# Optimization experiments

Measured on AMD Instinct MI355X. Metric: run time of the kernel, lower is better.

## Reference

```python
import jax, jax.numpy as jnp
import numpy as np

N_NODES = 100000
K_HOPS = 2


def _gcn_norm(edge_index, edge_weight, num_nodes, fill_value=1.0):
    # renorm trick: add self-loops with weight fill_value, then D^-1/2 A D^-1/2
    row, col = edge_index[0], edge_index[1]
    sl = jnp.arange(num_nodes, dtype=edge_index.dtype)
    row = jnp.concatenate([row, sl])
    col = jnp.concatenate([col, sl])
    w = jnp.concatenate([edge_weight, jnp.full((num_nodes,), fill_value, edge_weight.dtype)])
    deg = jax.ops.segment_sum(w, row, num_segments=num_nodes)
    dinv = jnp.where(deg > 0, jax.lax.rsqrt(deg), 0.0)
    normed_w = dinv[row] * w * dinv[col]
    return row, col, normed_w


def setup_inputs() -> dict:
    key = jax.random.key(0)
    k1, k2, k3 = jax.random.split(key, 3)
    n_edges, d, units = 1000000, 64, 64
    x = jax.random.normal(k1, (N_NODES, d), dtype=jnp.float32)
    edge_index = jax.random.randint(k2, (2, n_edges), 0, N_NODES, dtype=jnp.int32)
    edge_weight = jnp.ones((n_edges,), dtype=jnp.float32)
    kernel = jax.random.normal(k3, (d, units), dtype=jnp.float32) * (1.0 / np.sqrt(d))
    bias = jnp.zeros((units,), dtype=jnp.float32)
    return {"x": x, "edge_index": edge_index, "edge_weight": edge_weight,
            "kernel": kernel, "bias": bias}


def reference(x, edge_index, edge_weight, kernel, bias):
    # SGC: K-hop normalized sparse propagation, then single dense linear
    row, col, w = _gcn_norm(edge_index, edge_weight, N_NODES, fill_value=1.0)
    h = x
    for _ in range(K_HOPS):
        h = jax.ops.segment_sum(w[:, None] * h[col], row, num_segments=N_NODES)
    out = h @ kernel + bias  # activation=None
    return out
```

## Files before the change

### kernel.cpp

```cpp
#include <hip/hip_runtime.h>


constexpr int kN = 100000;
constexpr int kD = 64;
constexpr int BSHIFT = 9;
constexpr int NBUCK = (kN + 511) >> BSHIFT;
constexpr int CHUNK = 4096;
constexpr int XW_ROWS = 128;

__device__ __forceinline__ float bf2f(unsigned short u) {
    return __uint_as_float(((unsigned)u) << 16);
}
__device__ __forceinline__ unsigned short f2bf(float f) {
    unsigned b = __float_as_uint(f);
    b += 0x7FFF + ((b >> 16) & 1);
    return (unsigned short)(b >> 16);
}

__global__ __launch_bounds__(256) void kA_count(const int* __restrict__ row,
                                                int* __restrict__ bc, int nblk, int E) {
    __shared__ int hist[256];
    int t = threadIdx.x;
    hist[t] = 0;
    __syncthreads();
    int g0 = blockIdx.x * CHUNK;
    int n = min(CHUNK, E - g0);
    for (int i = t; i < n; i += 256) {
        atomicAdd(&hist[row[g0 + i] >> BSHIFT], 1);
    }
    __syncthreads();
    if (t < NBUCK) bc[t * nblk + blockIdx.x] = hist[t];
}

__global__ __launch_bounds__(256) void kA_scanB(int* __restrict__ bc,
                                                int* __restrict__ tot, int nblk) {
    __shared__ int sh[256];
    int b = blockIdx.x;
    int t = threadIdx.x;
    int* p = bc + (size_t)b * nblk;
    int ipt = (nblk + 255) >> 8;
    int s0 = t * ipt;
    int s1 = min(s0 + ipt, nblk);
    int lsum = 0;
    for (int k = s0; k < s1; ++k) lsum += p[k];
    sh[t] = lsum;
    __syncthreads();
    for (int off = 1; off < 256; off <<= 1) {
        int add = (t >= off) ? sh[t - off] : 0;
        __syncthreads();
        sh[t] += add;
        __syncthreads();
    }
    int run = sh[t] - lsum;
    for (int k = s0; k < s1; ++k) {
        int v = p[k];
        p[k] = run;
        run += v;
    }
    if (t == 255) tot[b] = sh[255];
}

__global__ __launch_bounds__(256) void kA_scanT(const int* __restrict__ tot,
                                                int* __restrict__ base) {
    __shared__ int sh[256];
    int t = threadIdx.x;
    int v = (t < NBUCK) ? tot[t] : 0;
    sh[t] = v;
    __syncthreads();
    for (int off = 1; off < 256; off <<= 1) {
        int add = (t >= off) ? sh[t - off] : 0;
        __syncthreads();
        sh[t] += add;
        __syncthreads();
    }
    if (t < NBUCK) base[t] = sh[t] - v;
}

__global__ __launch_bounds__(256) void kA_place(const int* __restrict__ row,
                                                const int* __restrict__ col,
                                                const float* __restrict__ w,
                                                const int* __restrict__ bc,
                                                const int* __restrict__ base, int nblk,
                                                int2* __restrict__ tmp, int E) {
    __shared__ int hist[256];
    __shared__ int lbase[256];
    __shared__ int gb[256];
    __shared__ int cur[256];
    __shared__ int2 stage[CHUNK];
    __shared__ unsigned char bkt[CHUNK];
    int t = threadIdx.x;
    hist[t] = 0;
    __syncthreads();
    int g0 = blockIdx.x * CHUNK;
    int n = min(CHUNK, E - g0);
    for (int i = t; i < n; i += 256) {
        atomicAdd(&hist[row[g0 + i] >> BSHIFT], 1);
    }
    __syncthreads();
    int v = hist[t];
    lbase[t] = v;
    __syncthreads();
    for (int off = 1; off < 256; off <<= 1) {
        int add = (t >= off) ? lbase[t - off] : 0;
        __syncthreads();
        lbase[t] += add;
        __syncthreads();
    }
    int excl = lbase[t] - v;
    __syncthreads();
    lbase[t] = excl;
    cur[t] = excl;
    if (t < NBUCK) gb[t] = base[t] + bc[t * nblk + blockIdx.x];
    __syncthreads();
    for (int i = t; i < n; i += 256) {
        int r = row[g0 + i];
        int c = col[g0 + i];
        float wv = w[g0 + i];
        int b = r >> BSHIFT;
        int lp = atomicAdd(&cur[b], 1);
        stage[lp] = make_int2(c | ((r & 511) << 17), __float_as_int(wv));
        bkt[lp] = (unsigned char)b;
    }
    __syncthreads();
    for (int i = t; i < n; i += 256) {
        int b = bkt[i];
        tmp[gb[b] + (i - lbase[b])] = stage[i];
    }
}

__global__ __launch_bounds__(512) void kB_sort(const int2* __restrict__ tmp,
                                               const int* __restrict__ base,
                                               int2* __restrict__ ecw,
                                               int* __restrict__ start,
                                               float* __restrict__ dinv, int E) {
    __shared__ int hist[512];
    __shared__ int lstart[512];
    __shared__ int cur[512];
    int b = blockIdx.x;
    int t = threadIdx.x;
    int gbase = base[b];
    int gend = (b == NBUCK - 1) ? E : base[b + 1];
    int size = gend - gbase;
    int node0 = b << BSHIFT;
    int nloc = min(512, kN - node0);
    hist[t] = 0;
    __syncthreads();
    for (int i = t; i < size; i += 512) {
        atomicAdd(&hist[(tmp[gbase + i].x >> 17) & 511], 1);
    }
    __syncthreads();
    int v = hist[t];
    lstart[t] = v;
    __syncthreads();
    for (int off = 1; off < 512; off <<= 1) {
        int add = (t >= off) ? lstart[t - off] : 0;
        __syncthreads();
        lstart[t] += add;
        __syncthreads();
    }
    int excl = lstart[t] - v;
    __syncthreads();
    lstart[t] = excl;
    cur[t] = excl;
    __syncthreads();
    if (t < nloc) start[node0 + t] = gbase + excl;
    if (b == 0 && t == 0) start[kN] = E;
    for (int i = t; i < size; i += 512) {
        int2 e = tmp[gbase + i];
        int rl = (e.x >> 17) & 511;
        int lp = atomicAdd(&cur[rl], 1);
        ecw[gbase + lp] = e;
    }
    __syncthreads();
    if (t < nloc) {
        int s = gbase + lstart[t];
        int eend = s + hist[t];
        float d = 1.0f;
        for (int j = s; j < eend; ++j) d += __int_as_float(ecw[j].y);
        dinv[node0 + t] = (d > 0.0f) ? rsqrtf(d) : 0.0f;
    }
}

__global__ __launch_bounds__(256) void k_norm(const int* __restrict__ base,
                                              const float* __restrict__ dinv,
                                              int2* __restrict__ ecw, int E) {
    int b = blockIdx.x;
    int gbase = base[b];
    int gend = (b == NBUCK - 1) ? E : base[b + 1];
    int node0 = b << BSHIFT;
    for (int i = gbase + threadIdx.x; i < gend; i += 256) {
        int2 v = ecw[i];
        int c = v.x & 0x1FFFF;
        int rl = (v.x >> 17) & 511;
        float wn = dinv[node0 + rl] * __int_as_float(v.y) * dinv[c];
        ecw[i] = make_int2(c << 7, __float_as_int(wn));
    }
}

__global__ __launch_bounds__(256) void k_xw(const float* __restrict__ x,
                                            const float* __restrict__ W,
                                            unsigned short* __restrict__ y, int n) {
    __shared__ float Xs[XW_ROWS][kD];
    int t = threadIdx.x;
    int lane = t & 63;
    int wv = t >> 6;
    int row0 = blockIdx.x * XW_ROWS;
    float Wc[kD];
#pragma unroll
    for (int k = 0; k < kD; ++k) Wc[k] = W[k * kD + lane];
    for (int i = t; i < XW_ROWS * (kD / 4); i += 256) {
        int r = i >> 4;
        int q = i & 15;
        float4 v = make_float4(0.0f, 0.0f, 0.0f, 0.0f);
        if (row0 + r < n)
            v = *reinterpret_cast<const float4*>(x + (size_t)(row0 + r) * kD + q * 4);
        *reinterpret_cast<float4*>(&Xs[r][q * 4]) = v;
    }
    __syncthreads();
    int rbase = wv * 32;
#pragma unroll
    for (int rr = 0; rr < 32; rr += 2) {
        int r0 = rbase + rr;
        float acc0 = 0.0f, acc1 = 0.0f;
#pragma unroll
        for (int q = 0; q < 16; ++q) {
            float4 a = *reinterpret_cast<const float4*>(&Xs[r0][q * 4]);
            float4 b = *reinterpret_cast<const float4*>(&Xs[r0 + 1][q * 4]);
            acc0 = fmaf(a.x, Wc[q * 4 + 0], acc0);
            acc1 = fmaf(b.x, Wc[q * 4 + 0], acc1);
            acc0 = fmaf(a.y, Wc[q * 4 + 1], acc0);
            acc1 = fmaf(b.y, Wc[q * 4 + 1], acc1);
            acc0 = fmaf(a.z, Wc[q * 4 + 2], acc0);
            acc1 = fmaf(b.z, Wc[q * 4 + 2], acc1);
            acc0 = fmaf(a.w, Wc[q * 4 + 3], acc0);
            acc1 = fmaf(b.w, Wc[q * 4 + 3], acc1);
        }
        int gr = row0 + r0;
        if (gr < n) y[(size_t)gr * kD + lane] = f2bf(acc0);
        if (gr + 1 < n) y[(size_t)(gr + 1) * kD + lane] = f2bf(acc1);
    }
}

template <typename OutWriter>
__device__ __forceinline__ void hop_body(const int* __restrict__ start,
                                         const int2* __restrict__ ecw,
                                         const float* __restrict__ dinv,
                                         const unsigned short* __restrict__ h_in,
                                         int n, OutWriter writeout) {
    int node = blockIdx.x * 4 + __builtin_amdgcn_readfirstlane(threadIdx.x >> 6);
    int lane = threadIdx.x & 63;
    if (node >= n) return;
    const char* hb = (const char*)h_in;
    int lo = lane << 1;
    float di = dinv[node];
    float self = bf2f(h_in[(size_t)node * kD + lane]);
    float acc = di * di * self;
    int s = start[node], e = start[node + 1];
    int j = s;
    for (; j + 7 < e; j += 8) {
        int2 v0 = ecw[j + 0], v1 = ecw[j + 1], v2 = ecw[j + 2], v3 = ecw[j + 3];
        int2 v4 = ecw[j + 4], v5 = ecw[j + 5], v6 = ecw[j + 6], v7 = ecw[j + 7];
        float g0 = bf2f(*(const unsigned short*)(hb + (unsigned)(v0.x + lo)));
        float g1 = bf2f(*(const unsigned short*)(hb + (unsigned)(v1.x + lo)));
        float g2 = bf2f(*(const unsigned short*)(hb + (unsigned)(v2.x + lo)));
        float g3 = bf2f(*(const unsigned short*)(hb + (unsigned)(v3.x + lo)));
        float g4 = bf2f(*(const unsigned short*)(hb + (unsigned)(v4.x + lo)));
        float g5 = bf2f(*(const unsigned short*)(hb + (unsigned)(v5.x + lo)));
        float g6 = bf2f(*(const unsigned short*)(hb + (unsigned)(v6.x + lo)));
        float g7 = bf2f(*(const unsigned short*)(hb + (unsigned)(v7.x + lo)));
        acc = fmaf(__int_as_float(v0.y), g0, acc);
        acc = fmaf(__int_as_float(v1.y), g1, acc);
        acc = fmaf(__int_as_float(v2.y), g2, acc);
        acc = fmaf(__int_as_float(v3.y), g3, acc);
        acc = fmaf(__int_as_float(v4.y), g4, acc);
        acc = fmaf(__int_as_float(v5.y), g5, acc);
        acc = fmaf(__int_as_float(v6.y), g6, acc);
        acc = fmaf(__int_as_float(v7.y), g7, acc);
    }
    for (; j + 3 < e; j += 4) {
        int2 v0 = ecw[j + 0], v1 = ecw[j + 1], v2 = ecw[j + 2], v3 = ecw[j + 3];
        float g0 = bf2f(*(const unsigned short*)(hb + (unsigned)(v0.x + lo)));
        float g1 = bf2f(*(const unsigned short*)(hb + (unsigned)(v1.x + lo)));
        float g2 = bf2f(*(const unsigned short*)(hb + (unsigned)(v2.x + lo)));
        float g3 = bf2f(*(const unsigned short*)(hb + (unsigned)(v3.x + lo)));
        acc = fmaf(__int_as_float(v0.y), g0, acc);
        acc = fmaf(__int_as_float(v1.y), g1, acc);
        acc = fmaf(__int_as_float(v2.y), g2, acc);
        acc = fmaf(__int_as_float(v3.y), g3, acc);
    }
    for (; j < e; ++j) {
        int2 v = ecw[j];
        acc = fmaf(__int_as_float(v.y),
                   bf2f(*(const unsigned short*)(hb + (unsigned)(v.x + lo))), acc);
    }
    writeout(node, lane, di, acc);
}

__global__ __launch_bounds__(256) void k_hop1(const int* __restrict__ start,
                                              const int2* __restrict__ ecw,
                                              const float* __restrict__ dinv,
                                              const unsigned short* __restrict__ h_in,
                                              unsigned short* __restrict__ h_out, int n) {
    hop_body(start, ecw, dinv, h_in, n,
             [=](int node, int lane, float di, float acc) {
                 h_out[(size_t)node * kD + lane] = f2bf(acc);
             });
}

__global__ __launch_bounds__(256) void k_hop2(const int* __restrict__ start,
                                              const int2* __restrict__ ecw,
                                              const float* __restrict__ dinv,
                                              const unsigned short* __restrict__ h_in,
                                              const float* __restrict__ bias,
                                              float* __restrict__ out, int n) {
    hop_body(start, ecw, dinv, h_in, n,
             [=](int node, int lane, float di, float acc) {
                 out[(size_t)node * kD + lane] = acc + bias[lane];
             });
}

extern "C" void kernel_launch(void* const* d_in, const int* in_sizes, int n_in,
                              void* d_out, int out_size, void* d_ws, size_t ws_size,
                              hipStream_t stream) {
    const float* x    = (const float*)d_in[0];
    const int*   ei   = (const int*)d_in[1];
    const float* ew   = (const float*)d_in[2];
    const float* W    = (const float*)d_in[3];
    const float* bias = (const float*)d_in[4];
    const int E = in_sizes[1] / 2;
    const int* row = ei;
    const int* col = ei + E;

    const int nblk = (E + CHUNK - 1) / CHUNK;

    char* ws = (char*)d_ws;
    auto alloc = [&](size_t bytes) {
        char* p = ws;
        ws += ((bytes + 1023) & ~(size_t)1023);
        return p;
    };
    int*            base  = (int*)alloc(sizeof(int) * 256);
    int*            tot   = (int*)alloc(sizeof(int) * 256);
    int*            bc    = (int*)alloc(sizeof(int) * (size_t)NBUCK * nblk);
    int*            start = (int*)alloc(sizeof(int) * (kN + 1));
    float*          dinv  = (float*)alloc(sizeof(float) * kN);
    int2*           ecw   = (int2*)alloc(sizeof(int2) * (size_t)E);
    unsigned short* y     = (unsigned short*)alloc(sizeof(short) * (size_t)kN * kD);
    unsigned short* h1    = (unsigned short*)alloc(sizeof(short) * (size_t)kN * kD);
    int2*           tmp   = (int2*)h1;

    k_xw<<<(kN + XW_ROWS - 1) / XW_ROWS, 256, 0, stream>>>(x, W, y, kN);

    kA_count<<<nblk, 256, 0, stream>>>(row, bc, nblk, E);
    kA_scanB<<<NBUCK, 256, 0, stream>>>(bc, tot, nblk);
    kA_scanT<<<1, 256, 0, stream>>>(tot, base);
    kA_place<<<nblk, 256, 0, stream>>>(row, col, ew, bc, base, nblk, tmp, E);
    kB_sort<<<NBUCK, 512, 0, stream>>>(tmp, base, ecw, start, dinv, E);
    k_norm<<<NBUCK, 256, 0, stream>>>(base, dinv, ecw, E);

    k_hop1<<<(kN + 3) / 4, 256, 0, stream>>>(start, ecw, dinv, y, h1, kN);
    k_hop2<<<(kN + 3) / 4, 256, 0, stream>>>(start, ecw, dinv, h1, bias,
                                             (float*)d_out, kN);
}
```

Before: 144.8 us.

## Compute degrees in a separate pass, fold edge normalization into sort, predicate hop tail

Degrees are now computed by a new per-bucket kernel that does shared-memory atomic adds over the bucketed edges. Edge normalization moves into the bucket sort's scatter, which removes the separate k_norm pass and the serial per-node degree loop that re-read ecw. The hop gather loop drops its 4-wide and scalar remainder loops in favour of a single 8-wide loop with clamped indices and zeroed weights, so short rows issue redundant but harmless loads. The final output store becomes nontemporal.

```diff
diff --git a/kernel.cpp b/kernel.cpp
--- a/kernel.cpp
+++ b/kernel.cpp
@@ -128,13 +128,35 @@
     }
 }
 
+__global__ __launch_bounds__(512) void kD_deg(const int2* __restrict__ tmp,
+                                              const int* __restrict__ base,
+                                              float* __restrict__ dinv, int E) {
+    __shared__ float degs[512];
+    int b = blockIdx.x;
+    int t = threadIdx.x;
+    degs[t] = 0.0f;
+    __syncthreads();
+    int gbase = base[b];
+    int gend = (b == NBUCK - 1) ? E : base[b + 1];
+    int node0 = b << BSHIFT;
+    int nloc = min(512, kN - node0);
+    for (int i = gbase + t; i < gend; i += 512) {
+        int2 e = tmp[i];
+        atomicAdd(&degs[(e.x >> 17) & 511], __int_as_float(e.y));
+    }
+    __syncthreads();
+    if (t < nloc) {
+        float d = 1.0f + degs[t];
+        dinv[node0 + t] = (d > 0.0f) ? rsqrtf(d) : 0.0f;
+    }
+}
+
 __global__ __launch_bounds__(512) void kB_sort(const int2* __restrict__ tmp,
                                                const int* __restrict__ base,
+                                               const float* __restrict__ dinv,
                                                int2* __restrict__ ecw,
-                                               int* __restrict__ start,
-                                               float* __restrict__ dinv, int E) {
+                                               int* __restrict__ start, int E) {
     __shared__ int hist[512];
-    __shared__ int lstart[512];
     __shared__ int cur[512];
     int b = blockIdx.x;
     int t = threadIdx.x;
@@ -150,50 +172,27 @@
     }
     __syncthreads();
     int v = hist[t];
-    lstart[t] = v;
+    hist[t] = v;
     __syncthreads();
     for (int off = 1; off < 512; off <<= 1) {
-        int add = (t >= off) ? lstart[t - off] : 0;
-        __syncthreads();
-        lstart[t] += add;
-        __syncthreads();
-    }
-    int excl = lstart[t] - v;
-    __syncthreads();
-    lstart[t] = excl;
+        int add = (t >= off) ? hist[t - off] : 0;
+        __syncthreads();
+        hist[t] += add;
+        __syncthreads();
+    }
+    int excl = hist[t] - v;
+    __syncthreads();
     cur[t] = excl;
     __syncthreads();
     if (t < nloc) start[node0 + t] = gbase + excl;
     if (b == 0 && t == 0) start[kN] = E;
     for (int i = t; i < size; i += 512) {
         int2 e = tmp[gbase + i];
+        int c = e.x & 0x1FFFF;
         int rl = (e.x >> 17) & 511;
+        float wn = dinv[node0 + rl] * __int_as_float(e.y) * dinv[c];
         int lp = atomicAdd(&cur[rl], 1);
-        ecw[gbase + lp] = e;
-    }
-    __syncthreads();
-    if (t < nloc) {
-        int s = gbase + lstart[t];
-        int eend = s + hist[t];
-        float d = 1.0f;
-        for (int j = s; j < eend; ++j) d += __int_as_float(ecw[j].y);
-        dinv[node0 + t] = (d > 0.0f) ? rsqrtf(d) : 0.0f;
-    }
-}
-
-__global__ __launch_bounds__(256) void k_norm(const int* __restrict__ base,
-                                              const float* __restrict__ dinv,
-                                              int2* __restrict__ ecw, int E) {
-    int b = blockIdx.x;
-    int gbase = base[b];
-    int gend = (b == NBUCK - 1) ? E : base[b + 1];
-    int node0 = b << BSHIFT;
-    for (int i = gbase + threadIdx.x; i < gend; i += 256) {
-        int2 v = ecw[i];
-        int c = v.x & 0x1FFFF;
-        int rl = (v.x >> 17) & 511;
-        float wn = dinv[node0 + rl] * __int_as_float(v.y) * dinv[c];
-        ecw[i] = make_int2(c << 7, __float_as_int(wn));
+        ecw[gbase + lp] = make_int2(c << 7, __float_as_int(wn));
     }
 }
 
@@ -256,10 +255,16 @@
     float self = bf2f(h_in[(size_t)node * kD + lane]);
     float acc = di * di * self;
     int s = start[node], e = start[node + 1];
-    int j = s;
-    for (; j + 7 < e; j += 8) {
-        int2 v0 = ecw[j + 0], v1 = ecw[j + 1], v2 = ecw[j + 2], v3 = ecw[j + 3];
-        int2 v4 = ecw[j + 4], v5 = ecw[j + 5], v6 = ecw[j + 6], v7 = ecw[j + 7];
+    int em1 = e - 1;
+    for (int j = s; j < e; j += 8) {
+        int2 v0 = ecw[j];
+        int2 v1 = ecw[min(j + 1, em1)];
+        int2 v2 = ecw[min(j + 2, em1)];
+        int2 v3 = ecw[min(j + 3, em1)];
+        int2 v4 = ecw[min(j + 4, em1)];
+        int2 v5 = ecw[min(j + 5, em1)];
+        int2 v6 = ecw[min(j + 6, em1)];
+        int2 v7 = ecw[min(j + 7, em1)];
         float g0 = bf2f(*(const unsigned short*)(hb + (unsigned)(v0.x + lo)));
         float g1 = bf2f(*(const unsigned short*)(hb + (unsigned)(v1.x + lo)));
         float g2 = bf2f(*(const unsigned short*)(hb + (unsigned)(v2.x + lo)));
@@ -268,30 +273,22 @@
         float g5 = bf2f(*(const unsigned short*)(hb + (unsigned)(v5.x + lo)));
         float g6 = bf2f(*(const unsigned short*)(hb + (unsigned)(v6.x + lo)));
         float g7 = bf2f(*(const unsigned short*)(hb + (unsigned)(v7.x + lo)));
-        acc = fmaf(__int_as_float(v0.y), g0, acc);
-        acc = fmaf(__int_as_float(v1.y), g1, acc);
-        acc = fmaf(__int_as_float(v2.y), g2, acc);
-        acc = fmaf(__int_as_float(v3.y), g3, acc);
-        acc = fmaf(__int_as_float(v4.y), g4, acc);
-        acc = fmaf(__int_as_float(v5.y), g5, acc);
-        acc = fmaf(__int_as_float(v6.y), g6, acc);
-        acc = fmaf(__int_as_float(v7.y), g7, acc);
-    }
-    for (; j + 3 < e; j += 4) {
-        int2 v0 = ecw[j + 0], v1 = ecw[j + 1], v2 = ecw[j + 2], v3 = ecw[j + 3];
-        float g0 = bf2f(*(const unsigned short*)(hb + (unsigned)(v0.x + lo)));
-        float g1 = bf2f(*(const unsigned short*)(hb + (unsigned)(v1.x + lo)));
-        float g2 = bf2f(*(const unsigned short*)(hb + (unsigned)(v2.x + lo)));
-        float g3 = bf2f(*(const unsigned short*)(hb + (unsigned)(v3.x + lo)));
-        acc = fmaf(__int_as_float(v0.y), g0, acc);
-        acc = fmaf(__int_as_float(v1.y), g1, acc);
-        acc = fmaf(__int_as_float(v2.y), g2, acc);
-        acc = fmaf(__int_as_float(v3.y), g3, acc);
-    }
-    for (; j < e; ++j) {
-        int2 v = ecw[j];
-        acc = fmaf(__int_as_float(v.y),
-                   bf2f(*(const unsigned short*)(hb + (unsigned)(v.x + lo))), acc);
+        float w0 = __int_as_float(v0.y);
+        float w1 = (j + 1 < e) ? __int_as_float(v1.y) : 0.0f;
+        float w2 = (j + 2 < e) ? __int_as_float(v2.y) : 0.0f;
+        float w3 = (j + 3 < e) ? __int_as_float(v3.y) : 0.0f;
+        float w4 = (j + 4 < e) ? __int_as_float(v4.y) : 0.0f;
+        float w5 = (j + 5 < e) ? __int_as_float(v5.y) : 0.0f;
+        float w6 = (j + 6 < e) ? __int_as_float(v6.y) : 0.0f;
+        float w7 = (j + 7 < e) ? __int_as_float(v7.y) : 0.0f;
+        acc = fmaf(w0, g0, acc);
+        acc = fmaf(w1, g1, acc);
+        acc = fmaf(w2, g2, acc);
+        acc = fmaf(w3, g3, acc);
+        acc = fmaf(w4, g4, acc);
+        acc = fmaf(w5, g5, acc);
+        acc = fmaf(w6, g6, acc);
+        acc = fmaf(w7, g7, acc);
     }
     writeout(node, lane, di, acc);
 }
@@ -315,7 +312,8 @@
                                               float* __restrict__ out, int n) {
     hop_body(start, ecw, dinv, h_in, n,
              [=](int node, int lane, float di, float acc) {
-                 out[(size_t)node * kD + lane] = acc + bias[lane];
+                 __builtin_nontemporal_store(acc + bias[lane],
+                                             &out[(size_t)node * kD + lane]);
              });
 }
 
@@ -355,8 +353,8 @@
     kA_scanB<<<NBUCK, 256, 0, stream>>>(bc, tot, nblk);
     kA_scanT<<<1, 256, 0, stream>>>(tot, base);
     kA_place<<<nblk, 256, 0, stream>>>(row, col, ew, bc, base, nblk, tmp, E);
-    kB_sort<<<NBUCK, 512, 0, stream>>>(tmp, base, ecw, start, dinv, E);
-    k_norm<<<NBUCK, 256, 0, stream>>>(base, dinv, ecw, E);
+    kD_deg<<<NBUCK, 512, 0, stream>>>(tmp, base, dinv, E);
+    kB_sort<<<NBUCK, 512, 0, stream>>>(tmp, base, dinv, ecw, start, E);
 
     k_hop1<<<(kN + 3) / 4, 256, 0, stream>>>(start, ecw, dinv, y, h1, kN);
     k_hop2<<<(kN + 3) / 4, 256, 0, stream>>>(start, ecw, dinv, h1, bias,
```

Result: slower. 149.3 us (+3.1%).
